# Optimization experiments

Hardware: AMD Instinct MI355X
Metric: run time of the kernel (lower is better)

Reference implementation:

```python
import jax, jax.numpy as jnp
import numpy as np

jax.config.update("jax_enable_x64", True)

# Module constants (from MySDELayer.call / run_model)
NUM_TRAJ = 512
DT = 2.0 ** (-8)          # deltat
NSTEPS = 255              # len(arange(0,1,DT)) - 1
OMEGA = 5.0265            # params[0]
GAMMA = 0.36              # params[2]
SQG = float(np.sqrt(GAMMA))


def setup_inputs() -> dict:
    key = jax.random.key(0)
    k1, k2 = jax.random.split(key)
    inputs = jax.random.normal(k1, (32, 1), dtype=jnp.float32)
    # unit-normal Wiener increments; scaled by sqrt(DT) inside reference
    wvec = jax.random.normal(k2, (32 * NUM_TRAJ, NSTEPS, 2), dtype=jnp.float32)
    return {"inputs": inputs, "wvec": wvec}


def _sde_probs(eps, dw):
    """Euler-Maruyama integration of the Genois qubit heterodyne SDE in Bloch
    coordinates (d=3 state, m=2 Wiener channels, complex128 as in the original),
    followed by unwrap to rho and Pauli-expectation probabilities.
    eps: [N] complex128 (per-trajectory middle parameter, e.g. detuning)
    dw:  [N, NSTEPS, 2] complex128 Wiener increments (stddev sqrt(DT))
    returns probs [N, NSTEPS+1, 6] float64
    """
    N = eps.shape[0]
    x0 = jnp.broadcast_to(jnp.array([0.0, 0.0, 1.0], dtype=jnp.complex128), (N, 3))

    def step(x, dwt):  # x: [N,3], dwt: [N,2]
        xx, yy, zz = x[:, 0], x[:, 1], x[:, 2]
        # drift: Rabi drive OMEGA about x, detuning eps about z, dephasing GAMMA
        drift = jnp.stack([
            -eps * yy - GAMMA * xx,
            eps * xx - OMEGA * zz - GAMMA * yy,
            OMEGA * yy,
        ], axis=1)
        # heterodyne measurement backaction (two quadratures)
        b1 = SQG * jnp.stack([-xx * zz, -yy * zz, 1.0 - zz * zz], axis=1)
        b2 = SQG * jnp.stack([-yy, xx, jnp.zeros_like(xx)], axis=1)
        xn = x + drift * DT + b1 * dwt[:, 0:1] + b2 * dwt[:, 1:2]
        return xn, xn

    _, xs = jax.lax.scan(step, x0, jnp.swapaxes(dw, 0, 1))  # [NSTEPS, N, 3]
    xvec = jnp.concatenate([x0[None], xs], axis=0)           # [T, N, 3]
    xvec = jnp.transpose(xvec, (1, 0, 2))                    # [N, T, 3]

    # unwrap_x_to_rho: rho = 0.5*(I + r.sigma) as length-4 vec
    rho = jnp.stack([
        0.5 * (1.0 + xvec[..., 2]),
        0.5 * (xvec[..., 0] - 1j * xvec[..., 1]),
        0.5 * (xvec[..., 0] + 1j * xvec[..., 1]),
        0.5 * (1.0 - xvec[..., 2]),
    ], axis=-1)                                              # [N, T, 4]

    # calc_exp with Pauli matrices
    ex = jnp.real(rho[..., 1] + rho[..., 2])
    ey = jnp.real(1j * (rho[..., 1] - rho[..., 2]))
    ez = jnp.real(rho[..., 0] - rho[..., 3])
    px, py, pz = 0.5 * (ex + 1.0), 0.5 * (ey + 1.0), 0.5 * (ez + 1.0)
    return jnp.stack([px, 1.0 - px, py, 1.0 - py, pz, 1.0 - pz], axis=2)  # [N,T,6]


def reference(inputs, wvec):
    B = inputs.shape[0]
    # tf.tile(inputs, [num_traj, 1])[:, 0] -> trajectory-major replication
    eps = jnp.tile(inputs, (NUM_TRAJ, 1))[:, 0].astype(jnp.complex128)  # [N]
    dw = (wvec * np.sqrt(DT)).astype(jnp.complex128)                    # [N,255,2]
    probs = _sde_probs(eps, dw)                                         # [N,T,6]
    probs_by_params = probs.reshape(B, NUM_TRAJ, probs.shape[1], 6)
    return jnp.mean(probs_by_params, axis=1)                            # [B,T,6]
```

## Files before the change

### kernel.cpp

```cpp
#include <hip/hip_runtime.h>

#define NSTEPS 255
#define TPTS   256
#define NTRAJ  16384
#define NBLK   256
#define CH     15

#define GAMMA_F 0.36f
#define OMEGA_F 5.0265f
#define DT_F    0.00390625f
#define CW      0.0375f
#define GD      (GAMMA_F * DT_F)
#define OD      (OMEGA_F * DT_F)

#define PITCH  520
#define STATEB 132608

typedef __fp16 half2v __attribute__((ext_vector_type(2)));
typedef float  f32x2  __attribute__((ext_vector_type(2)));

__device__ __forceinline__ unsigned pk2(float a, float b) {
  half2v h = __builtin_amdgcn_cvt_pkrtz(a, b);
  return __builtin_bit_cast(unsigned, h);
}

#define STEP2(wx_, wy_, ii_) {                                                  \
  const float w0  = (wx_) * CW;                                                 \
  const float cy  = (wy_) * CW;                                                 \
  const f32x2 sw  = __builtin_shufflevector(v, v, 1, 0);             \
  f32x2 t = __builtin_elementwise_fma(epack, sw, v);                            \
  t = __builtin_elementwise_fma(mGD2, v, t);                                    \
  const f32x2 w0s = {w0, w0};                             \
  t = __builtin_elementwise_fma(-(v * z), w0s, t);               \
  const f32x2 cys = {-cy, cy};                                 \
  t = __builtin_elementwise_fma(sw, cys, t);                                    \
  t[1] = __builtin_fmaf(-OD, z, t[1]);                                          \
  const float a_ = __builtin_fmaf(OD, v[1], z);                                 \
  const float r_ = __builtin_fmaf(-(z * z), w0, w0);                            \
  v = t; z = a_ + r_;                                                           \
  *(uint2*)(sb + (ii_) * PITCH) = make_uint2(pk2(v[0], v[1]), pk2(z, 0.0f));    \
}

#define LOADC(BUF, CHUNK_) {                                                    \
  _Pragma("unroll")                                                             \
  for (int i_ = 0; i_ < CH; ++i_) BUF[i_] = wrow[(CHUNK_) * CH + i_];           \
}

#define PROC(BUF) {                                                             \
  _Pragma("unroll")                                                             \
  for (int i_ = 0; i_ < CH; ++i_) STEP2((BUF)[i_].x, (BUF)[i_].y, i_)           \
  sb += CH * PITCH;                                                             \
}

__global__ __launch_bounds__(64) void sde_integrate(const float* __restrict__ inp,
                                                    const float* __restrict__ wvec,
                                                    float* __restrict__ partial) {
  __shared__ alignas(16) char smem[STATEB];
  const int g = blockIdx.x, l = threadIdx.x;
  const float eps = inp[l & 31];
  const f32x2 epack = {-eps * DT_F, eps * DT_F};
  const f32x2 mGD2  = {-GD, -GD};

  const float2* __restrict__ wrow =
      reinterpret_cast<const float2*>(wvec) + (size_t)(g * 64 + l) * NSTEPS;
  char* sb = smem + l * 8;

  f32x2 v = {0.0f, 0.0f};
  float z = 1.0f;

  float2 bufA[CH], bufB[CH], bufC[CH];

  LOADC(bufA, 0);
  LOADC(bufB, 1);
  #pragma unroll 1
  for (int k = 0; k < 5; ++k) {
    LOADC(bufC, 3 * k + 2); PROC(bufA);
    LOADC(bufA, 3 * k + 3); PROC(bufB);
    LOADC(bufB, 3 * k + 4); PROC(bufC);
  }
  PROC(bufA);
  PROC(bufB);

  __syncthreads();

  #pragma unroll
  for (int k = 0; k < 4; ++k) {
    const int s = l + 64 * k;
    if (s < NSTEPS) {
      const char* rb = smem + (size_t)s * PITCH;
      f32x2 sxy = {0.0f, 0.0f};
      float fz = 0.0f;
      #pragma unroll
      for (int j = 0; j < 64; ++j) {
        const uint2 u = *(const uint2*)(rb + j * 8);
        const half2v xy = __builtin_bit_cast(half2v, u.x);
        const half2v zp = __builtin_bit_cast(half2v, u.y);
        const f32x2 vxy = {(float)xy[0], (float)xy[1]};
        sxy += vxy;
        fz += (float)zp[0];
      }
      float* p = partial + ((size_t)g * NSTEPS + s) * 3;
      p[0] = sxy[0]; p[1] = sxy[1]; p[2] = fz;
    }
  }
}

__global__ __launch_bounds__(64) void sde_finalize(const float* __restrict__ partial,
                                                   float* __restrict__ out) {
  const int idx = blockIdx.x * 64 + threadIdx.x;
  const int b = idx >> 8;
  const int t = idx & 255;
  float* o = out + (size_t)idx * 6;

  if (t == 0) {
    o[0] = 0.5f; o[1] = 0.5f; o[2] = 0.5f; o[3] = 0.5f;
    o[4] = 1.0f; o[5] = 0.0f;
    return;
  }

  float sx = 0.0f, sy = 0.0f, sz = 0.0f;
  #pragma unroll
  for (int j = 0; j < 8; ++j) {
    const float* p = partial + ((size_t)(b * 8 + j) * NSTEPS + (t - 1)) * 3;
    sx += p[0]; sy += p[1]; sz += p[2];
  }
  const float inv = 1.0f / 512.0f;
  const float mx = sx * inv, my = sy * inv, mz = sz * inv;
  o[0] = 0.5f * (1.0f + mx);
  o[1] = 0.5f * (1.0f - mx);
  o[2] = 0.5f * (1.0f + my);
  o[3] = 0.5f * (1.0f - my);
  o[4] = 0.5f * (1.0f + mz);
  o[5] = 0.5f * (1.0f - mz);
}

extern "C" void kernel_launch(void* const* d_in, const int* in_sizes, int n_in,
                              void* d_out, int out_size, void* d_ws, size_t ws_size,
                              hipStream_t stream) {
  (void)in_sizes; (void)n_in; (void)out_size; (void)ws_size;
  const float* inp  = (const float*)d_in[0];
  const float* wvec = (const float*)d_in[1];
  float* out     = (float*)d_out;
  float* partial = (float*)d_ws;

  sde_integrate<<<NBLK, 64, 0, stream>>>(inp, wvec, partial);
  sde_finalize<<<128, 64, 0, stream>>>(partial, out);
}
```

Before: 22.99 us.

## Add producer warps staging coalesced Wiener tiles through shared memory

Launches 256 threads per block. Three producer wavefronts load the Wiener increments with coalesced reads into a triple-buffered, swizzled shared-memory tile, while one compute wavefront runs the serial Euler-Maruyama recurrence from LDS. The old version had each thread issue strided per-row global loads. The final reduction over trajectories is now spread across all 256 threads instead of one wavefront looping four times. The cost is 16 block-wide barriers that serialize the compute wave with the producers, plus extra LDS traffic and larger shared memory use.

```diff
diff --git a/kernel.cpp b/kernel.cpp
--- a/kernel.cpp
+++ b/kernel.cpp
@@ -1,10 +1,9 @@
 #include <hip/hip_runtime.h>
 
 #define NSTEPS 255
-#define TPTS   256
 #define NTRAJ  16384
 #define NBLK   256
-#define CH     15
+#define ROWB   2040
 
 #define GAMMA_F 0.36f
 #define OMEGA_F 5.0265f
@@ -15,6 +14,8 @@
 
 #define PITCH  520
 #define STATEB 132608
+
+#define TILEB  8192
 
 typedef __fp16 half2v __attribute__((ext_vector_type(2)));
 typedef float  f32x2  __attribute__((ext_vector_type(2)));
@@ -30,9 +31,9 @@
   const f32x2 sw  = __builtin_shufflevector(v, v, 1, 0);             \
   f32x2 t = __builtin_elementwise_fma(epack, sw, v);                            \
   t = __builtin_elementwise_fma(mGD2, v, t);                                    \
-  const f32x2 w0s = {w0, w0};                             \
-  t = __builtin_elementwise_fma(-(v * z), w0s, t);               \
-  const f32x2 cys = {-cy, cy};                                 \
+  const f32x2 w0s = {w0, w0};                                                   \
+  t = __builtin_elementwise_fma(-(v * z), w0s, t);                              \
+  const f32x2 cys = {-cy, cy};                                                  \
   t = __builtin_elementwise_fma(sw, cys, t);                                    \
   t[1] = __builtin_fmaf(-OD, z, t[1]);                                          \
   const float a_ = __builtin_fmaf(OD, v[1], z);                                 \
@@ -41,67 +42,98 @@
   *(uint2*)(sb + (ii_) * PITCH) = make_uint2(pk2(v[0], v[1]), pk2(z, 0.0f));    \
 }
 
-#define LOADC(BUF, CHUNK_) {                                                    \
+#define PLOAD(R, c) {                                                           \
   _Pragma("unroll")                                                             \
-  for (int i_ = 0; i_ < CH; ++i_) BUF[i_] = wrow[(CHUNK_) * CH + i_];           \
+  for (int i_ = 0; i_ < 6; ++i_) {                                              \
+    const int e_ = p + 192 * i_;                                                \
+    if (e_ < 1024 && ((c) < 15 || (e_ & 15) < 15))                              \
+      R[i_] = *(const float2*)(wbase + (size_t)(e_ >> 4) * ROWB                 \
+                               + (size_t)(c) * 128 + (e_ & 15) * 8);            \
+  }                                                                             \
 }
 
-#define PROC(BUF) {                                                             \
+#define PWRITE(R, c) {                                                          \
+  char* const tb_ = tiles + ((c) % 3) * TILEB;                                  \
   _Pragma("unroll")                                                             \
-  for (int i_ = 0; i_ < CH; ++i_) STEP2((BUF)[i_].x, (BUF)[i_].y, i_)           \
-  sb += CH * PITCH;                                                             \
+  for (int i_ = 0; i_ < 6; ++i_) {                                              \
+    const int e_ = p + 192 * i_;                                                \
+    if (e_ < 1024 && ((c) < 15 || (e_ & 15) < 15)) {                            \
+      const int r_ = e_ >> 4, c0_ = e_ & 15;                                    \
+      *(float2*)(tb_ + r_ * 128 + (((c0_ + r_) & 15) * 8)) = R[i_];             \
+    }                                                                           \
+  }                                                                             \
 }
 
-__global__ __launch_bounds__(64) void sde_integrate(const float* __restrict__ inp,
-                                                    const float* __restrict__ wvec,
-                                                    float* __restrict__ partial) {
-  __shared__ alignas(16) char smem[STATEB];
-  const int g = blockIdx.x, l = threadIdx.x;
+#define CCHUNK(k_, NK) {                                                        \
+  const char* tb_ = tiles + ((k_) % 3) * TILEB + l * 128;                       \
+  _Pragma("unroll")                                                             \
+  for (int p_ = 0; p_ < (NK); ++p_) {                                           \
+    const float2 w2 = *(const float2*)(tb_ + (((p_ + l) & 15) * 8));            \
+    STEP2(w2.x, w2.y, p_);                                                      \
+  }                                                                             \
+  sb += (NK) * PITCH;                                                           \
+}
+
+__global__ __launch_bounds__(256) void sde_integrate(const float* __restrict__ inp,
+                                                     const float* __restrict__ wvec,
+                                                     float* __restrict__ partial) {
+  __shared__ alignas(16) char smem[STATEB + 3 * TILEB];
+  char* const tiles = smem + STATEB;
+  const int g   = blockIdx.x;
+  const int tid = threadIdx.x;
+  const int wid = tid >> 6;
+  const int l   = tid & 63;
+  const int p   = tid - 64;
+
   const float eps = inp[l & 31];
   const f32x2 epack = {-eps * DT_F, eps * DT_F};
   const f32x2 mGD2  = {-GD, -GD};
-
-  const float2* __restrict__ wrow =
-      reinterpret_cast<const float2*>(wvec) + (size_t)(g * 64 + l) * NSTEPS;
   char* sb = smem + l * 8;
-
   f32x2 v = {0.0f, 0.0f};
   float z = 1.0f;
 
-  float2 bufA[CH], bufB[CH], bufC[CH];
+  const char* wbase = (const char*)wvec + (size_t)g * 64 * ROWB;
+  float2 rA[6] = {}, rB[6] = {};
 
-  LOADC(bufA, 0);
-  LOADC(bufB, 1);
-  #pragma unroll 1
-  for (int k = 0; k < 5; ++k) {
-    LOADC(bufC, 3 * k + 2); PROC(bufA);
-    LOADC(bufA, 3 * k + 3); PROC(bufB);
-    LOADC(bufB, 3 * k + 4); PROC(bufC);
+  if (wid > 0) {
+    PLOAD(rA, 0);
+    PLOAD(rB, 1);
+    PWRITE(rA, 0);
+    PLOAD(rA, 2);
+    PWRITE(rB, 1);
   }
-  PROC(bufA);
-  PROC(bufB);
-
   __syncthreads();
 
-  #pragma unroll
-  for (int k = 0; k < 4; ++k) {
-    const int s = l + 64 * k;
-    if (s < NSTEPS) {
-      const char* rb = smem + (size_t)s * PITCH;
-      f32x2 sxy = {0.0f, 0.0f};
-      float fz = 0.0f;
-      #pragma unroll
-      for (int j = 0; j < 64; ++j) {
-        const uint2 u = *(const uint2*)(rb + j * 8);
-        const half2v xy = __builtin_bit_cast(half2v, u.x);
-        const half2v zp = __builtin_bit_cast(half2v, u.y);
-        const f32x2 vxy = {(float)xy[0], (float)xy[1]};
-        sxy += vxy;
-        fz += (float)zp[0];
+  #pragma unroll 1
+  for (int k = 0; k < 16; ++k) {
+    if (wid > 0) {
+      if (k + 2 < 16) {
+        if (k & 1) { PWRITE(rB, k + 2); if (k + 3 < 16) PLOAD(rA, k + 3); }
+        else       { PWRITE(rA, k + 2); if (k + 3 < 16) PLOAD(rB, k + 3); }
       }
-      float* p = partial + ((size_t)g * NSTEPS + s) * 3;
-      p[0] = sxy[0]; p[1] = sxy[1]; p[2] = fz;
+    } else {
+      if (k < 15) { CCHUNK(k, 16); }
+      else        { CCHUNK(k, 15); }
     }
+    __syncthreads();
+  }
+
+  const int s = tid;
+  if (s < NSTEPS) {
+    const char* rb = smem + (size_t)s * PITCH;
+    f32x2 sxy = {0.0f, 0.0f};
+    float fz = 0.0f;
+    #pragma unroll
+    for (int j = 0; j < 64; ++j) {
+      const uint2 u = *(const uint2*)(rb + j * 8);
+      const half2v xy = __builtin_bit_cast(half2v, u.x);
+      const half2v zp = __builtin_bit_cast(half2v, u.y);
+      const f32x2 vxy = {(float)xy[0], (float)xy[1]};
+      sxy += vxy;
+      fz += (float)zp[0];
+    }
+    float* pp = partial + ((size_t)g * NSTEPS + s) * 3;
+    pp[0] = sxy[0]; pp[1] = sxy[1]; pp[2] = fz;
   }
 }
 
@@ -121,8 +153,8 @@
   float sx = 0.0f, sy = 0.0f, sz = 0.0f;
   #pragma unroll
   for (int j = 0; j < 8; ++j) {
-    const float* p = partial + ((size_t)(b * 8 + j) * NSTEPS + (t - 1)) * 3;
-    sx += p[0]; sy += p[1]; sz += p[2];
+    const float* pp = partial + ((size_t)(b * 8 + j) * NSTEPS + (t - 1)) * 3;
+    sx += pp[0]; sy += pp[1]; sz += pp[2];
   }
   const float inv = 1.0f / 512.0f;
   const float mx = sx * inv, my = sy * inv, mz = sz * inv;
@@ -143,6 +175,6 @@
   float* out     = (float*)d_out;
   float* partial = (float*)d_ws;
 
-  sde_integrate<<<NBLK, 64, 0, stream>>>(inp, wvec, partial);
+  sde_integrate<<<NBLK, 256, 0, stream>>>(inp, wvec, partial);
   sde_finalize<<<128, 64, 0, stream>>>(partial, out);
 }
```

Measured after the change: 32.17 us. +39.9%, slower.

## Fuse finalize into integrate kernel via per-group atomic counter; shorten step dependency chain

Applied to the files above, without the earlier changes.

Removes the separate finalize launch. Each block bumps a per-batch atomic counter after writing its partials, and the last of the 8 blocks in a group reduces them and writes the output. The Euler step is also reorganized into independent terms summed at the end, which shortens the serial FMA chain on the state. In exchange it relies on the workspace counters starting in a consistent state, since they are never reset and only modulo arithmetic keeps repeated calls correct, and it adds fence and atomic overhead.

```diff
diff --git a/kernel.cpp b/kernel.cpp
--- a/kernel.cpp
+++ b/kernel.cpp
@@ -1,7 +1,6 @@
 #include <hip/hip_runtime.h>
 
 #define NSTEPS 255
-#define TPTS   256
 #define NTRAJ  16384
 #define NBLK   256
 #define CH     15
@@ -16,6 +15,8 @@
 #define PITCH  520
 #define STATEB 132608
 
+#define PARTB  783360
+
 typedef __fp16 half2v __attribute__((ext_vector_type(2)));
 typedef float  f32x2  __attribute__((ext_vector_type(2)));
 
@@ -25,16 +26,16 @@
 }
 
 #define STEP2(wx_, wy_, ii_) {                                                  \
-  const float w0  = (wx_) * CW;                                                 \
-  const float cy  = (wy_) * CW;                                                 \
-  const f32x2 sw  = __builtin_shufflevector(v, v, 1, 0);             \
-  f32x2 t = __builtin_elementwise_fma(epack, sw, v);                            \
-  t = __builtin_elementwise_fma(mGD2, v, t);                                    \
-  const f32x2 w0s = {w0, w0};                             \
-  t = __builtin_elementwise_fma(-(v * z), w0s, t);               \
-  const f32x2 cys = {-cy, cy};                                 \
-  t = __builtin_elementwise_fma(sw, cys, t);                                    \
-  t[1] = __builtin_fmaf(-OD, z, t[1]);                                          \
+  const float w0 = (wx_) * CW;                                                  \
+  const float cy = (wy_) * CW;                                                  \
+  const f32x2 sw = __builtin_shufflevector(v, v, 1, 0);              \
+  const f32x2 term1 = __builtin_elementwise_fma(epack, sw, v);                  \
+  const f32x2 odz   = mOD2 * z;                                  \
+  const f32x2 term2 = __builtin_elementwise_fma(mGD2, v, odz);                  \
+  const f32x2 w0s = {w0, w0};                                                   \
+  const f32x2 cys = {-cy, cy};                                                  \
+  const f32x2 term3 = __builtin_elementwise_fma(-(v * z), w0s, sw * cys);       \
+  const f32x2 t = (term1 + term2) + term3;                                      \
   const float a_ = __builtin_fmaf(OD, v[1], z);                                 \
   const float r_ = __builtin_fmaf(-(z * z), w0, w0);                            \
   v = t; z = a_ + r_;                                                           \
@@ -54,12 +55,16 @@
 
 __global__ __launch_bounds__(64) void sde_integrate(const float* __restrict__ inp,
                                                     const float* __restrict__ wvec,
-                                                    float* __restrict__ partial) {
+                                                    float* __restrict__ partial,
+                                                    int* __restrict__ counters,
+                                                    float* __restrict__ out) {
   __shared__ alignas(16) char smem[STATEB];
+  __shared__ int sret;
   const int g = blockIdx.x, l = threadIdx.x;
   const float eps = inp[l & 31];
   const f32x2 epack = {-eps * DT_F, eps * DT_F};
   const f32x2 mGD2  = {-GD, -GD};
+  const f32x2 mOD2  = {0.0f, -OD};
 
   const float2* __restrict__ wrow =
       reinterpret_cast<const float2*>(wvec) + (size_t)(g * 64 + l) * NSTEPS;
@@ -103,35 +108,38 @@
       p[0] = sxy[0]; p[1] = sxy[1]; p[2] = fz;
     }
   }
-}
 
-__global__ __launch_bounds__(64) void sde_finalize(const float* __restrict__ partial,
-                                                   float* __restrict__ out) {
-  const int idx = blockIdx.x * 64 + threadIdx.x;
-  const int b = idx >> 8;
-  const int t = idx & 255;
-  float* o = out + (size_t)idx * 6;
+  __threadfence();
+  if (l == 0) sret = atomicAdd(counters + (g >> 3), 1);
+  __syncthreads();
+  if ((sret & 7) != 7) return;
+  __threadfence();
 
-  if (t == 0) {
-    o[0] = 0.5f; o[1] = 0.5f; o[2] = 0.5f; o[3] = 0.5f;
-    o[4] = 1.0f; o[5] = 0.0f;
-    return;
+  const int grp = g >> 3;
+  #pragma unroll
+  for (int k = 0; k < 4; ++k) {
+    const int t = l + 64 * k;
+    float* o = out + ((size_t)grp * 256 + t) * 6;
+    if (t == 0) {
+      o[0] = 0.5f; o[1] = 0.5f; o[2] = 0.5f; o[3] = 0.5f;
+      o[4] = 1.0f; o[5] = 0.0f;
+    } else {
+      float sx = 0.0f, sy = 0.0f, sz = 0.0f;
+      #pragma unroll
+      for (int j = 0; j < 8; ++j) {
+        const float* p = partial + ((size_t)(grp * 8 + j) * NSTEPS + (t - 1)) * 3;
+        sx += p[0]; sy += p[1]; sz += p[2];
+      }
+      const float inv = 1.0f / 512.0f;
+      const float mx = sx * inv, my = sy * inv, mz = sz * inv;
+      o[0] = 0.5f * (1.0f + mx);
+      o[1] = 0.5f * (1.0f - mx);
+      o[2] = 0.5f * (1.0f + my);
+      o[3] = 0.5f * (1.0f - my);
+      o[4] = 0.5f * (1.0f + mz);
+      o[5] = 0.5f * (1.0f - mz);
+    }
   }
-
-  float sx = 0.0f, sy = 0.0f, sz = 0.0f;
-  #pragma unroll
-  for (int j = 0; j < 8; ++j) {
-    const float* p = partial + ((size_t)(b * 8 + j) * NSTEPS + (t - 1)) * 3;
-    sx += p[0]; sy += p[1]; sz += p[2];
-  }
-  const float inv = 1.0f / 512.0f;
-  const float mx = sx * inv, my = sy * inv, mz = sz * inv;
-  o[0] = 0.5f * (1.0f + mx);
-  o[1] = 0.5f * (1.0f - mx);
-  o[2] = 0.5f * (1.0f + my);
-  o[3] = 0.5f * (1.0f - my);
-  o[4] = 0.5f * (1.0f + mz);
-  o[5] = 0.5f * (1.0f - mz);
 }
 
 extern "C" void kernel_launch(void* const* d_in, const int* in_sizes, int n_in,
@@ -140,9 +148,9 @@
   (void)in_sizes; (void)n_in; (void)out_size; (void)ws_size;
   const float* inp  = (const float*)d_in[0];
   const float* wvec = (const float*)d_in[1];
-  float* out     = (float*)d_out;
-  float* partial = (float*)d_ws;
+  float* out      = (float*)d_out;
+  float* partial  = (float*)d_ws;
+  int*   counters = (int*)((char*)d_ws + PARTB);
 
-  sde_integrate<<<NBLK, 64, 0, stream>>>(inp, wvec, partial);
-  sde_finalize<<<128, 64, 0, stream>>>(partial, out);
+  sde_integrate<<<NBLK, 64, 0, stream>>>(inp, wvec, partial, counters, out);
 }
```

Result: slower. 30.31 us (+31.8%).

## Integrate two trajectories per thread with half-size blocks and two-pass LDS reduction

Applied to the files above, without the earlier changes.

Each thread now integrates two independent trajectories, one from each half of the trajectory range, interleaving their dependent SDE steps to expose instruction-level parallelism. The grid is halved to 128 blocks. The per-step history buffer covers only 128 steps, so the reduction runs in two passes with extra barriers, which shrinks shared memory per block. The cost is half as many wavefronts across the GPU, more registers per thread, and more synchronization, while the long serial dependency chain per trajectory is hidden better.

```diff
diff --git a/kernel.cpp b/kernel.cpp
--- a/kernel.cpp
+++ b/kernel.cpp
@@ -1,10 +1,9 @@
 #include <hip/hip_runtime.h>
 
 #define NSTEPS 255
-#define TPTS   256
 #define NTRAJ  16384
-#define NBLK   256
-#define CH     15
+#define NBLK   128
+#define HALF   8192
 
 #define GAMMA_F 0.36f
 #define OMEGA_F 5.0265f
@@ -13,8 +12,8 @@
 #define GD      (GAMMA_F * DT_F)
 #define OD      (OMEGA_F * DT_F)
 
-#define PITCH  520
-#define STATEB 132608
+#define HPITCH 1032
+#define HBYTES (128 * HPITCH)
 
 typedef __fp16 half2v __attribute__((ext_vector_type(2)));
 typedef float  f32x2  __attribute__((ext_vector_type(2)));
@@ -24,85 +23,112 @@
   return __builtin_bit_cast(unsigned, h);
 }
 
-#define STEP2(wx_, wy_, ii_) {                                                  \
-  const float w0  = (wx_) * CW;                                                 \
-  const float cy  = (wy_) * CW;                                                 \
-  const f32x2 sw  = __builtin_shufflevector(v, v, 1, 0);             \
-  f32x2 t = __builtin_elementwise_fma(epack, sw, v);                            \
-  t = __builtin_elementwise_fma(mGD2, v, t);                                    \
-  const f32x2 w0s = {w0, w0};                             \
-  t = __builtin_elementwise_fma(-(v * z), w0s, t);               \
-  const f32x2 cys = {-cy, cy};                                 \
+#define STEP2(v_, z_, wx_, wy_, dst_) {                                         \
+  const float w0 = (wx_) * CW;                                                  \
+  const float cy = (wy_) * CW;                                                  \
+  const f32x2 sw = __builtin_shufflevector(v_, v_, 1, 0);            \
+  f32x2 t = __builtin_elementwise_fma(epack, sw, v_);                           \
+  t = __builtin_elementwise_fma(mGD2, v_, t);                                   \
+  const f32x2 w0s = {w0, w0};                                                   \
+  t = __builtin_elementwise_fma(-(v_ * z_), w0s, t);                            \
+  const f32x2 cys = {-cy, cy};                                                  \
   t = __builtin_elementwise_fma(sw, cys, t);                                    \
-  t[1] = __builtin_fmaf(-OD, z, t[1]);                                          \
-  const float a_ = __builtin_fmaf(OD, v[1], z);                                 \
-  const float r_ = __builtin_fmaf(-(z * z), w0, w0);                            \
-  v = t; z = a_ + r_;                                                           \
-  *(uint2*)(sb + (ii_) * PITCH) = make_uint2(pk2(v[0], v[1]), pk2(z, 0.0f));    \
+  t[1] = __builtin_fmaf(-OD, z_, t[1]);                                         \
+  const float a_ = __builtin_fmaf(OD, v_[1], z_);                               \
+  const float r_ = __builtin_fmaf(-(z_ * z_), w0, w0);                          \
+  v_ = t; z_ = a_ + r_;                                                         \
+  *(uint2*)(dst_) = make_uint2(pk2(v_[0], v_[1]), pk2(z_, 0.0f));               \
 }
 
-#define LOADC(BUF, CHUNK_) {                                                    \
+#define LOADC2(B0_, B1_, CH_, CNT) {                                            \
   _Pragma("unroll")                                                             \
-  for (int i_ = 0; i_ < CH; ++i_) BUF[i_] = wrow[(CHUNK_) * CH + i_];           \
+  for (int i_ = 0; i_ < (CNT); ++i_) {                                          \
+    B0_[i_] = wrow0[(CH_) * 16 + i_];                                           \
+    B1_[i_] = wrow1[(CH_) * 16 + i_];                                           \
+  }                                                                             \
 }
 
-#define PROC(BUF) {                                                             \
+#define PROC2(B0_, B1_, LSB, CNT) {                                             \
   _Pragma("unroll")                                                             \
-  for (int i_ = 0; i_ < CH; ++i_) STEP2((BUF)[i_].x, (BUF)[i_].y, i_)           \
-  sb += CH * PITCH;                                                             \
+  for (int i_ = 0; i_ < (CNT); ++i_) {                                          \
+    STEP2(v0, z0, (B0_)[i_].x, (B0_)[i_].y, hb + ((LSB) + i_) * HPITCH);        \
+    STEP2(v1, z1, (B1_)[i_].x, (B1_)[i_].y, hb + ((LSB) + i_) * HPITCH + 512);  \
+  }                                                                             \
+}
+
+#define TAILPASS(P, NS) {                                                       \
+  __syncthreads();                                                              \
+  _Pragma("unroll")                                                             \
+  for (int kk_ = 0; kk_ < 2; ++kk_) {                                           \
+    const int s_ = l + 64 * kk_;                                                \
+    if (s_ < (NS)) {                                                            \
+      const char* rb_ = hist + (size_t)s_ * HPITCH;                             \
+      f32x2 sxy0 = {0.0f, 0.0f}, sxy1 = {0.0f, 0.0f};                           \
+      float fz0 = 0.0f, fz1 = 0.0f;                                             \
+      _Pragma("unroll")                                                         \
+      for (int j_ = 0; j_ < 64; ++j_) {                                         \
+        const uint2 u0 = *(const uint2*)(rb_ + j_ * 8);                         \
+        const uint2 u1 = *(const uint2*)(rb_ + 512 + j_ * 8);                   \
+        const half2v xy0 = __builtin_bit_cast(half2v, u0.x);                    \
+        const half2v zp0 = __builtin_bit_cast(half2v, u0.y);                    \
+        const half2v xy1 = __builtin_bit_cast(half2v, u1.x);                    \
+        const half2v zp1 = __builtin_bit_cast(half2v, u1.y);                    \
+        const f32x2 a0 = {(float)xy0[0], (float)xy0[1]};                        \
+        const f32x2 a1 = {(float)xy1[0], (float)xy1[1]};                        \
+        sxy0 += a0; fz0 += (float)zp0[0];                                       \
+        sxy1 += a1; fz1 += (float)zp1[0];                                       \
+      }                                                                         \
+      const int row_ = (P) * 128 + s_;                                          \
+      float* p0_ = partial + ((size_t)g * NSTEPS + row_) * 3;                   \
+      float* p1_ = partial + ((size_t)(128 + g) * NSTEPS + row_) * 3;           \
+      p0_[0] = sxy0[0]; p0_[1] = sxy0[1]; p0_[2] = fz0;                         \
+      p1_[0] = sxy1[0]; p1_[1] = sxy1[1]; p1_[2] = fz1;                         \
+    }                                                                           \
+  }                                                                             \
+  __syncthreads();                                                              \
 }
 
 __global__ __launch_bounds__(64) void sde_integrate(const float* __restrict__ inp,
                                                     const float* __restrict__ wvec,
                                                     float* __restrict__ partial) {
-  __shared__ alignas(16) char smem[STATEB];
+  __shared__ alignas(16) char hist[HBYTES];
   const int g = blockIdx.x, l = threadIdx.x;
   const float eps = inp[l & 31];
   const f32x2 epack = {-eps * DT_F, eps * DT_F};
   const f32x2 mGD2  = {-GD, -GD};
 
-  const float2* __restrict__ wrow =
+  const float2* __restrict__ wrow0 =
       reinterpret_cast<const float2*>(wvec) + (size_t)(g * 64 + l) * NSTEPS;
-  char* sb = smem + l * 8;
+  const float2* __restrict__ wrow1 =
+      reinterpret_cast<const float2*>(wvec) + (size_t)(HALF + g * 64 + l) * NSTEPS;
+  char* const hb = hist + l * 8;
 
-  f32x2 v = {0.0f, 0.0f};
-  float z = 1.0f;
+  f32x2 v0 = {0.0f, 0.0f}, v1 = {0.0f, 0.0f};
+  float z0 = 1.0f, z1 = 1.0f;
 
-  float2 bufA[CH], bufB[CH], bufC[CH];
+  float2 A0[16], A1[16], B0[16], B1[16];
 
-  LOADC(bufA, 0);
-  LOADC(bufB, 1);
+  LOADC2(A0, A1, 0, 16);
   #pragma unroll 1
-  for (int k = 0; k < 5; ++k) {
-    LOADC(bufC, 3 * k + 2); PROC(bufA);
-    LOADC(bufA, 3 * k + 3); PROC(bufB);
-    LOADC(bufB, 3 * k + 4); PROC(bufC);
+  for (int k = 0; k < 4; ++k) {
+    LOADC2(B0, B1, 2 * k + 1, 16);
+    PROC2(A0, A1, 32 * k, 16);
+    LOADC2(A0, A1, 2 * k + 2, 16);
+    PROC2(B0, B1, 32 * k + 16, 16);
   }
-  PROC(bufA);
-  PROC(bufB);
+  TAILPASS(0, 128);
 
-  __syncthreads();
-
-  #pragma unroll
-  for (int k = 0; k < 4; ++k) {
-    const int s = l + 64 * k;
-    if (s < NSTEPS) {
-      const char* rb = smem + (size_t)s * PITCH;
-      f32x2 sxy = {0.0f, 0.0f};
-      float fz = 0.0f;
-      #pragma unroll
-      for (int j = 0; j < 64; ++j) {
-        const uint2 u = *(const uint2*)(rb + j * 8);
-        const half2v xy = __builtin_bit_cast(half2v, u.x);
-        const half2v zp = __builtin_bit_cast(half2v, u.y);
-        const f32x2 vxy = {(float)xy[0], (float)xy[1]};
-        sxy += vxy;
-        fz += (float)zp[0];
-      }
-      float* p = partial + ((size_t)g * NSTEPS + s) * 3;
-      p[0] = sxy[0]; p[1] = sxy[1]; p[2] = fz;
-    }
+  #pragma unroll 1
+  for (int k = 0; k < 3; ++k) {
+    LOADC2(B0, B1, 2 * k + 9, 16);
+    PROC2(A0, A1, 32 * k, 16);
+    LOADC2(A0, A1, 2 * k + 10, 16);
+    PROC2(B0, B1, 32 * k + 16, 16);
   }
+  LOADC2(B0, B1, 15, 15);
+  PROC2(A0, A1, 96, 16);
+  PROC2(B0, B1, 112, 15);
+  TAILPASS(1, 127);
 }
 
 __global__ __launch_bounds__(64) void sde_finalize(const float* __restrict__ partial,
```

New measurement: 35.54 us. 54.6% more time.
